# Optimization experiments

Hardware: AMD Instinct MI355X
Metric: run time of the kernel (lower is better)

Reference implementation:

```python
import jax, jax.numpy as jnp
import numpy as np

B, CIN, COUT, K, H, W = 16, 256, 256, 3, 64, 64
COND = 512


def setup_inputs() -> dict:
    key = jax.random.key(0)
    ks = jax.random.split(key, 10)
    X = jax.random.normal(ks[0], (B, CIN, H, W), dtype=jnp.float32)
    cond_v = jax.random.normal(ks[1], (B, COND), dtype=jnp.float32)
    # conv weight [O, I, kh, kw]
    conv_w = jax.random.normal(ks[2], (COUT, CIN, K, K), dtype=jnp.float32) / np.sqrt(CIN * K * K)
    w0 = jax.random.normal(ks[3], (COND, COND), dtype=jnp.float32) / np.sqrt(COND)
    b0 = jnp.zeros((COND,), dtype=jnp.float32)
    w1 = jax.random.normal(ks[4], (COND, COND), dtype=jnp.float32) / np.sqrt(COND)
    b1 = jnp.zeros((COND,), dtype=jnp.float32)
    w_out = jax.random.normal(ks[5], (CIN, COND), dtype=jnp.float32) / np.sqrt(COND)
    b_out = jnp.zeros((CIN,), dtype=jnp.float32)
    return {"X": X, "cond_v": cond_v, "conv_w": conv_w,
            "w0": w0, "b0": b0, "w1": w1, "b1": b1,
            "w_out": w_out, "b_out": b_out}


def reference(X, cond_v, conv_w, w0, b0, w1, b1, w_out, b_out):
    # proj_cond MLP: (Linear+SiLU) x depth, final Linear -> in_channels
    h = jax.nn.silu(cond_v @ w0.T + b0)
    h = jax.nn.silu(h @ w1.T + b1)
    scale = h @ w_out.T + b_out + 1.0          # [B, I]
    # modulate: bw[b,o,i,kh,kw] = w[o,i,kh,kw] * scale[b,i]
    bw = conv_w[None] * scale[:, None, :, None, None]
    # demodulate across (i, kh, kw)
    demod = jax.lax.rsqrt(jnp.sum(bw * bw, axis=(2, 3, 4)) + 1e-8)  # [B, O]
    bw = bw * demod[:, :, None, None, None]
    b, o, i, kh, kw = bw.shape
    # per-sample conv via grouped conv: x -> [1, B*I, H, W], w -> [B*O, I, kh, kw]
    x = X.reshape(1, b * i, X.shape[2], X.shape[3])
    w = bw.reshape(b * o, i, kh, kw)
    out = jax.lax.conv_general_dilated(
        x, w, window_strides=(1, 1), padding="SAME",
        feature_group_count=b,
        dimension_numbers=("NCHW", "OIHW", "NCHW"))
    return out.reshape(b, o, out.shape[2], out.shape[3])
```

## Files before the change

### kernel.cpp

```cpp
#include <hip/hip_runtime.h>
#include <hip/hip_bf16.h>
#include <cstdint>

#define NB 16
#define CI 256
#define CO 256
#define HH 64
#define WW 64
#define CC 512
#define HP 66
#define WP 66

typedef short short8 __attribute__((ext_vector_type(8)));
typedef float floatx4 __attribute__((ext_vector_type(4)));
typedef unsigned int uintx4 __attribute__((ext_vector_type(4)));

__device__ __forceinline__ void g2lds16(const void* g, void* l) {
  __builtin_amdgcn_global_load_lds((const __attribute__((address_space(1))) void*)g,
                                   (__attribute__((address_space(3))) void*)l, 16, 0, 0);
}

#define ASM_VMCNT0() do { asm volatile("s_waitcnt vmcnt(0)" ::: "memory"); \
                          __builtin_amdgcn_sched_barrier(0); } while (0)
#define ASM_VMCNT4() do { asm volatile("s_waitcnt vmcnt(4)" ::: "memory"); \
                          __builtin_amdgcn_sched_barrier(0); } while (0)
#define RAW_BAR() do { __builtin_amdgcn_sched_barrier(0);  \
                       __builtin_amdgcn_s_barrier();       \
                       __builtin_amdgcn_sched_barrier(0); } while (0)

template<int KD, int N, bool SILU, bool PLUSONE, int BJ>
__global__ void k_mlp(const float* __restrict__ in, const float* __restrict__ w,
                      const float* __restrict__ bias, float* __restrict__ out) {
  __shared__ float4 sin4[KD / 4];
  const int nb = N / BJ;
  int b = blockIdx.x / nb;
  int j = (blockIdx.x % nb) * BJ + threadIdx.x;
  const float4* in4 = reinterpret_cast<const float4*>(in + (size_t)b * KD);
  for (int k = threadIdx.x; k < KD / 4; k += BJ) sin4[k] = in4[k];
  __syncthreads();
  float acc = bias[j];
  const float4* wr = reinterpret_cast<const float4*>(w + (size_t)j * KD);
#pragma unroll 8
  for (int kk = 0; kk < KD / 4; ++kk) {
    float4 wv = wr[kk];
    float4 sv = sin4[kk];
    acc += wv.x * sv.x + wv.y * sv.y + wv.z * sv.z + wv.w * sv.w;
  }
  if (SILU) acc = acc / (1.0f + __expf(-acc));
  if (PLUSONE) acc += 1.0f;
  out[(size_t)b * N + j] = acc;
}

__global__ void k_repack(const float* __restrict__ cw, __hip_bfloat16* __restrict__ Wt,
                         float* __restrict__ wsq) {
  int gid = blockIdx.x * 256 + threadIdx.x;
  if (gid >= CO * CI) return;
  const float* p = cw + (size_t)gid * 9;
  float s = 0.0f;
#pragma unroll
  for (int t = 0; t < 9; ++t) {
    float v = p[t];
    s += v * v;
    Wt[(size_t)t * CO * CI + gid] = __float2bfloat16(v);
  }
  wsq[gid] = s;
}

__global__ void k_demod(const float* __restrict__ wsq, const float* __restrict__ scale,
                        float* __restrict__ demod) {
  __shared__ float s2[CI];
  int b = blockIdx.x;
  int o = threadIdx.x;
  float sv = scale[b * CI + o];
  s2[o] = sv * sv;
  __syncthreads();
  float acc = 0.0f;
  const float4* wr = reinterpret_cast<const float4*>(wsq + (size_t)o * CI);
  const float4* s4 = reinterpret_cast<const float4*>(s2);
#pragma unroll 8
  for (int i = 0; i < CI / 4; ++i) {
    float4 wv = wr[i];
    float4 sq = s4[i];
    acc += wv.x * sq.x + wv.y * sq.y + wv.z * sq.z + wv.w * sq.w;
  }
  demod[b * CO + o] = rsqrtf(acc + 1e-8f);
}

__global__ void k_scalex(const float* __restrict__ X, const float* __restrict__ scale,
                         __hip_bfloat16* __restrict__ Xs) {
  __shared__ float tile[64][68];
  __shared__ float ssc[64];
  int bid = blockIdx.x;
  int b = bid >> 8;
  int rem = bid & 255;
  int h = rem >> 2;
  int i0 = (rem & 3) * 64;
  int t = threadIdx.x;
  if (t < 64) ssc[t] = scale[b * CI + i0 + t];

  __hip_bfloat16* xs_img = Xs + (size_t)b * HP * WP * CI;
  uintx4 z = {0u, 0u, 0u, 0u};
  if (t < 16) {
    int px = (t >> 3) * 65;
    int sl = t & 7;
    *reinterpret_cast<uintx4*>(xs_img + (((size_t)(h + 1)) * WP + px) * CI + i0 + sl * 8) = z;
  }
  if (h == 0) {
    for (int u = t; u < 66 * 8; u += 256) {
      int px = u >> 3, sl = u & 7;
      *reinterpret_cast<uintx4*>(xs_img + ((size_t)px) * CI + i0 + sl * 8) = z;
    }
  }
  if (h == 63) {
    for (int u = t; u < 66 * 8; u += 256) {
      int px = u >> 3, sl = u & 7;
      *reinterpret_cast<uintx4*>(xs_img + ((size_t)65 * WP + px) * CI + i0 + sl * 8) = z;
    }
  }

  const float* src = X + (((size_t)b * CI + i0) * HH + h) * WW;
  int ii_base = t >> 4;
  int w4 = (t & 15) * 4;
#pragma unroll
  for (int r2 = 0; r2 < 4; ++r2) {
    int ii = r2 * 16 + ii_base;
    int key = ((ii >> 3) & 7) << 2;
    *reinterpret_cast<float4*>(&tile[ii][w4 ^ key]) =
        *reinterpret_cast<const float4*>(src + (size_t)ii * HH * WW + w4);
  }
  __syncthreads();
  int u = t & 7;
  int wl = t >> 3;
  int key = u << 2;
#pragma unroll
  for (int iter = 0; iter < 2; ++iter) {
    int w2 = wl + iter * 32;
    union { unsigned short us[8]; uintx4 v; } pk;
#pragma unroll
    for (int j = 0; j < 8; ++j) {
      int ii = u * 8 + j;
      float v = tile[ii][w2 ^ key] * ssc[ii];
      __hip_bfloat16 hb = __float2bfloat16(v);
      pk.us[j] = *reinterpret_cast<unsigned short*>(&hb);
    }
    *reinterpret_cast<uintx4*>(xs_img + (((size_t)(h + 1)) * WP + (w2 + 1)) * CI + i0 + u * 8) = pk.v;
  }
}

__global__ __launch_bounds__(512, 2)
void k_conv(const __hip_bfloat16* __restrict__ Xs, const __hip_bfloat16* __restrict__ Wt,
            const float* __restrict__ demod, float* __restrict__ out) {
  __shared__ __align__(16) char lds[55296 + 2 * 32768];
  char* sX  = lds;
  char* sA0 = lds + 55296;

  int wg = (blockIdx.x & 7) * 32 + (blockIdx.x >> 3);
  int b = wg >> 4;
  int ht = wg & 15;
  int h0 = ht * 4;

  int tid = threadIdx.x;
  int wv = tid >> 6;
  int lane = tid & 63;
  int lhi = lane >> 4;
  int llo = lane & 15;
  int wo = wv >> 1;
  int wpx = wv & 1;

  floatx4 acc[4][8];
#pragma unroll
  for (int m = 0; m < 4; ++m)
#pragma unroll
    for (int n = 0; n < 8; ++n) acc[m][n] = (floatx4){0.f, 0.f, 0.f, 0.f};

  int row_a[4], ra7[4];
#pragma unroll
  for (int m = 0; m < 4; ++m) { row_a[m] = wo * 64 + m * 16 + llo; ra7[m] = row_a[m] & 7; }

  const __hip_bfloat16* xs_img = Xs + (size_t)b * HP * WP * CI;

  for (int ic = 0; ic < 4; ++ic) {
    for (int j = wv; j < 54; j += 8) {
      int u = j * 64 + lane;
      int pr = u >> 3;
      int slot = lane & 7;
      int lr = pr / 72;
      int wp = pr - lr * 72;
      if (wp > 65) wp = 65;
      int isel = ic * 64 + ((slot ^ (pr & 7)) << 3);
      const __hip_bfloat16* src = xs_img + (((size_t)(h0 + lr) * WP + wp) * CI + isel);
      g2lds16(src, sX + j * 1024);
    }
    {
      const __hip_bfloat16* wbase = Wt + ic * 64;
#pragma unroll
      for (int jj = 0; jj < 4; ++jj) {
        int j = wv * 4 + jj;
        int row = j * 8 + (lane >> 3);
        int slot = lane & 7;
        int isel = (slot ^ (row & 7)) << 3;
        g2lds16(wbase + (size_t)row * CI + isel, sA0 + j * 1024);
      }
    }
    ASM_VMCNT0();
    RAW_BAR();

    for (int t = 0; t < 9; ++t) {
      char* sA = sA0 + (t & 1) * 32768;
      if (t < 8) {
        const __hip_bfloat16* wbase = Wt + (size_t)(t + 1) * CO * CI + ic * 64;
        char* dst = sA0 + ((t + 1) & 1) * 32768;
#pragma unroll
        for (int jj = 0; jj < 4; ++jj) {
          int j = wv * 4 + jj;
          int row = j * 8 + (lane >> 3);
          int slot = lane & 7;
          int isel = (slot ^ (row & 7)) << 3;
          g2lds16(wbase + (size_t)row * CI + isel, dst + j * 1024);
        }
        ASM_VMCNT4();
      } else {
        ASM_VMCNT0();
      }
      RAW_BAR();

      int kh = t / 3;
      int kw = t - kh * 3;
#pragma unroll
      for (int k32 = 0; k32 < 2; ++k32) {
        int kidx = k32 * 4 + lhi;
        short8 af[4];
#pragma unroll
        for (int m = 0; m < 4; ++m) {
          int addr = row_a[m] * 128 + ((kidx ^ ra7[m]) << 4);
          af[m] = *reinterpret_cast<const short8*>(sA + addr);
        }
#pragma unroll
        for (int n = 0; n < 8; ++n) {
          int stripe = wpx * 2 + (n >> 2) + kh;
          int px = (n & 3) * 16 + llo + kw;
          int prl = stripe * 72 + px;
          int addr = prl * 128 + ((kidx ^ (prl & 7)) << 4);
          short8 bq = *reinterpret_cast<const short8*>(sX + addr);
#pragma unroll
          for (int m = 0; m < 4; ++m)
            acc[m][n] = __builtin_amdgcn_mfma_f32_16x16x32_bf16(af[m], bq, acc[m][n], 0, 0, 0);
        }
      }
      RAW_BAR();
    }
  }

#pragma unroll
  for (int m = 0; m < 4; ++m) {
    int obase_o = wo * 64 + m * 16 + lhi * 4;
    float4 dmv = *reinterpret_cast<const float4*>(demod + (size_t)b * CO + obase_o);
#pragma unroll
    for (int j = 0; j < 4; ++j) {
      int o = obase_o + j;
      float dm = (j == 0) ? dmv.x : (j == 1) ? dmv.y : (j == 2) ? dmv.z : dmv.w;
      float* orow = out + (((size_t)b * CO + o) * HH + h0) * WW;
#pragma unroll
      for (int n = 0; n < 8; ++n) {
        int row = wpx * 2 + (n >> 2);
        int col = (n & 3) * 16 + llo;
        orow[(size_t)row * WW + col] = acc[m][n][j] * dm;
      }
    }
  }
}

extern "C" void kernel_launch(void* const* d_in, const int* in_sizes, int n_in,
                              void* d_out, int out_size, void* d_ws, size_t ws_size,
                              hipStream_t stream) {
  const float* X      = (const float*)d_in[0];
  const float* cond_v = (const float*)d_in[1];
  const float* conv_w = (const float*)d_in[2];
  const float* w0     = (const float*)d_in[3];
  const float* b0     = (const float*)d_in[4];
  const float* w1     = (const float*)d_in[5];
  const float* b1     = (const float*)d_in[6];
  const float* w_out  = (const float*)d_in[7];
  const float* b_out  = (const float*)d_in[8];
  float* out = (float*)d_out;

  char* ws = (char*)d_ws;
  const size_t XS_BYTES  = (size_t)NB * HP * WP * CI * 2;
  const size_t WT_BYTES  = (size_t)9 * CO * CI * 2;
  const size_t WSQ_BYTES = (size_t)CO * CI * 4;
  __hip_bfloat16* Xs = (__hip_bfloat16*)ws;
  __hip_bfloat16* Wt = (__hip_bfloat16*)(ws + XS_BYTES);
  float* wsq   = (float*)(ws + XS_BYTES + WT_BYTES);
  float* h0b   = (float*)(ws + XS_BYTES + WT_BYTES + WSQ_BYTES);
  float* h1b   = h0b + NB * CC;
  float* scale = h1b + NB * CC;
  float* demod = scale + NB * CI;

  k_repack<<<(CO * CI) / 256, 256, 0, stream>>>(conv_w, Wt, wsq);
  k_mlp<CC, CC, true, false, 128><<<NB * (CC / 128), 128, 0, stream>>>(cond_v, w0, b0, h0b);
  k_mlp<CC, CC, true, false, 128><<<NB * (CC / 128), 128, 0, stream>>>(h0b, w1, b1, h1b);
  k_mlp<CC, CI, false, true, 128><<<NB * (CI / 128), 128, 0, stream>>>(h1b, w_out, b_out, scale);
  k_demod<<<NB, CO, 0, stream>>>(wsq, scale, demod);
  k_scalex<<<NB * 64 * 4, 256, 0, stream>>>(X, scale, Xs);
  k_conv<<<NB * 16, 512, 0, stream>>>(Xs, Wt, demod, out);
}
```

Measured before the change: 135.9 us.

## Split conv over output-channel halves and double-buffer input tiles across 32-channel chunks

The conv kernel now launches twice as many 256-thread workgroups, each covering half of the output channels, and walks input channels in 32-wide chunks instead of 64. The X halo tile is double-buffered, and the next chunk's X is prefetched piecewise during the 9 tap iterations, so the per-chunk full drain and barrier before X reuse goes away. Weight tiles shrink to 8 KB double buffers. The aim is better load/compute overlap and more workgroups for occupancy. In exchange there are more barriers per MFMA (one k-step per tap instead of two), the X tile is reloaded by both output halves, and the XOR swizzle is dropped, which risks LDS bank conflicts.

```diff
diff --git a/kernel.cpp b/kernel.cpp
--- a/kernel.cpp
+++ b/kernel.cpp
@@ -22,7 +22,9 @@
 
 #define ASM_VMCNT0() do { asm volatile("s_waitcnt vmcnt(0)" ::: "memory"); \
                           __builtin_amdgcn_sched_barrier(0); } while (0)
-#define ASM_VMCNT4() do { asm volatile("s_waitcnt vmcnt(4)" ::: "memory"); \
+#define ASM_VMCNT2() do { asm volatile("s_waitcnt vmcnt(2)" ::: "memory"); \
+                          __builtin_amdgcn_sched_barrier(0); } while (0)
+#define ASM_VMCNT3() do { asm volatile("s_waitcnt vmcnt(3)" ::: "memory"); \
                           __builtin_amdgcn_sched_barrier(0); } while (0)
 #define RAW_BAR() do { __builtin_amdgcn_sched_barrier(0);  \
                        __builtin_amdgcn_s_barrier();       \
@@ -147,24 +149,27 @@
   }
 }
 
-__global__ __launch_bounds__(512, 2)
+__global__ __launch_bounds__(256, 2)
 void k_conv(const __hip_bfloat16* __restrict__ Xs, const __hip_bfloat16* __restrict__ Wt,
             const float* __restrict__ demod, float* __restrict__ out) {
-  __shared__ __align__(16) char lds[55296 + 2 * 32768];
-  char* sX  = lds;
-  char* sA0 = lds + 55296;
-
-  int wg = (blockIdx.x & 7) * 32 + (blockIdx.x >> 3);
-  int b = wg >> 4;
-  int ht = wg & 15;
+  __shared__ __align__(16) char lds[2 * 28672 + 2 * 8192];
+  char* sX0 = lds;
+  char* sA0 = lds + 57344;
+
+  int wg = (blockIdx.x & 7) * 64 + (blockIdx.x >> 3);
+  int b = wg >> 5;
+  int rem = wg & 31;
+  int ht = rem >> 1;
+  int ob = rem & 1;
   int h0 = ht * 4;
+  int o0 = ob * 128;
 
   int tid = threadIdx.x;
   int wv = tid >> 6;
   int lane = tid & 63;
   int lhi = lane >> 4;
   int llo = lane & 15;
-  int wo = wv >> 1;
+  int wo2 = wv >> 1;
   int wpx = wv & 1;
 
   floatx4 acc[4][8];
@@ -173,79 +178,72 @@
 #pragma unroll
     for (int n = 0; n < 8; ++n) acc[m][n] = (floatx4){0.f, 0.f, 0.f, 0.f};
 
-  int row_a[4], ra7[4];
-#pragma unroll
-  for (int m = 0; m < 4; ++m) { row_a[m] = wo * 64 + m * 16 + llo; ra7[m] = row_a[m] & 7; }
-
   const __hip_bfloat16* xs_img = Xs + (size_t)b * HP * WP * CI;
 
-  for (int ic = 0; ic < 4; ++ic) {
-    for (int j = wv; j < 54; j += 8) {
-      int u = j * 64 + lane;
-      int pr = u >> 3;
-      int slot = lane & 7;
-      int lr = pr / 72;
-      int wp = pr - lr * 72;
-      if (wp > 65) wp = 65;
-      int isel = ic * 64 + ((slot ^ (pr & 7)) << 3);
-      const __hip_bfloat16* src = xs_img + (((size_t)(h0 + lr) * WP + wp) * CI + isel);
-      g2lds16(src, sX + j * 1024);
-    }
-    {
-      const __hip_bfloat16* wbase = Wt + ic * 64;
-#pragma unroll
-      for (int jj = 0; jj < 4; ++jj) {
-        int j = wv * 4 + jj;
-        int row = j * 8 + (lane >> 3);
-        int slot = lane & 7;
-        int isel = (slot ^ (row & 7)) << 3;
-        g2lds16(wbase + (size_t)row * CI + isel, sA0 + j * 1024);
+  int xoff[7];
+#pragma unroll
+  for (int s = 0; s < 7; ++s) {
+    int j = wv + 4 * s;
+    int pr = 16 * j + (lane >> 2);
+    if (pr > 431) pr = 431;
+    int lr = pr / 72;
+    int wp = pr - lr * 72;
+    if (wp > 65) wp = 65;
+    xoff[s] = ((h0 + lr) * WP + wp) * CI + (lane & 3) * 8;
+  }
+  int a_off[2];
+#pragma unroll
+  for (int jj = 0; jj < 2; ++jj)
+    a_off[jj] = (o0 + 32 * wv + 16 * jj + (lane >> 2)) * CI + (lane & 3) * 8;
+
+#pragma unroll
+  for (int s = 0; s < 7; ++s)
+    g2lds16(xs_img + xoff[s], sX0 + (wv + 4 * s) * 1024);
+#pragma unroll
+  for (int jj = 0; jj < 2; ++jj)
+    g2lds16(Wt + a_off[jj], sA0 + (wv * 2 + jj) * 1024);
+  ASM_VMCNT0();
+  RAW_BAR();
+
+  for (int c = 0; c < 8; ++c) {
+    const char* xbuf = sX0 + (c & 1) * 28672;
+#pragma unroll
+    for (int t = 0; t < 9; ++t) {
+      int gt = c * 9 + t;
+      bool xiss = (t >= 2) && (c < 7);
+      if (xiss) {
+        int s = t - 2;
+        g2lds16(xs_img + xoff[s] + (c + 1) * 32,
+                sX0 + ((c + 1) & 1) * 28672 + (wv + 4 * s) * 1024);
       }
-    }
-    ASM_VMCNT0();
-    RAW_BAR();
-
-    for (int t = 0; t < 9; ++t) {
-      char* sA = sA0 + (t & 1) * 32768;
-      if (t < 8) {
-        const __hip_bfloat16* wbase = Wt + (size_t)(t + 1) * CO * CI + ic * 64;
-        char* dst = sA0 + ((t + 1) & 1) * 32768;
-#pragma unroll
-        for (int jj = 0; jj < 4; ++jj) {
-          int j = wv * 4 + jj;
-          int row = j * 8 + (lane >> 3);
-          int slot = lane & 7;
-          int isel = (slot ^ (row & 7)) << 3;
-          g2lds16(wbase + (size_t)row * CI + isel, dst + j * 1024);
-        }
-        ASM_VMCNT4();
+      if (gt < 71) {
+        int nt = (t == 8) ? 0 : t + 1;
+        int ncc = (t == 8) ? c + 1 : c;
+        const __hip_bfloat16* wb = Wt + (size_t)nt * CO * CI + ncc * 32;
+        char* ad = sA0 + ((gt + 1) & 1) * 8192;
+        g2lds16(wb + a_off[0], ad + (wv * 2 + 0) * 1024);
+        g2lds16(wb + a_off[1], ad + (wv * 2 + 1) * 1024);
+        if (xiss) { ASM_VMCNT3(); } else { ASM_VMCNT2(); }
       } else {
         ASM_VMCNT0();
       }
       RAW_BAR();
 
+      const char* sA = sA0 + (gt & 1) * 8192;
       int kh = t / 3;
       int kw = t - kh * 3;
-#pragma unroll
-      for (int k32 = 0; k32 < 2; ++k32) {
-        int kidx = k32 * 4 + lhi;
-        short8 af[4];
-#pragma unroll
-        for (int m = 0; m < 4; ++m) {
-          int addr = row_a[m] * 128 + ((kidx ^ ra7[m]) << 4);
-          af[m] = *reinterpret_cast<const short8*>(sA + addr);
-        }
-#pragma unroll
-        for (int n = 0; n < 8; ++n) {
-          int stripe = wpx * 2 + (n >> 2) + kh;
-          int px = (n & 3) * 16 + llo + kw;
-          int prl = stripe * 72 + px;
-          int addr = prl * 128 + ((kidx ^ (prl & 7)) << 4);
-          short8 bq = *reinterpret_cast<const short8*>(sX + addr);
-#pragma unroll
-          for (int m = 0; m < 4; ++m)
-            acc[m][n] = __builtin_amdgcn_mfma_f32_16x16x32_bf16(af[m], bq, acc[m][n], 0, 0, 0);
-        }
+      short8 af[4];
+#pragma unroll
+      for (int m = 0; m < 4; ++m)
+        af[m] = *reinterpret_cast<const short8*>(sA + (wo2 * 64 + m * 16 + llo) * 64 + lhi * 16);
+#pragma unroll
+      for (int n = 0; n < 8; ++n) {
+        int stripe = wpx * 2 + (n >> 2) + kh;
+        int px = (n & 3) * 16 + llo + kw;
+        short8 bq = *reinterpret_cast<const short8*>(xbuf + (stripe * 72 + px) * 64 + lhi * 16);
+#pragma unroll
+        for (int m = 0; m < 4; ++m)
+          acc[m][n] = __builtin_amdgcn_mfma_f32_16x16x32_bf16(af[m], bq, acc[m][n], 0, 0, 0);
       }
       RAW_BAR();
     }
@@ -253,7 +251,7 @@
 
 #pragma unroll
   for (int m = 0; m < 4; ++m) {
-    int obase_o = wo * 64 + m * 16 + lhi * 4;
+    int obase_o = o0 + wo2 * 64 + m * 16 + lhi * 4;
     float4 dmv = *reinterpret_cast<const float4*>(demod + (size_t)b * CO + obase_o);
 #pragma unroll
     for (int j = 0; j < 4; ++j) {
@@ -302,5 +300,5 @@
   k_mlp<CC, CI, false, true, 128><<<NB * (CI / 128), 128, 0, stream>>>(h1b, w_out, b_out, scale);
   k_demod<<<NB, CO, 0, stream>>>(wsq, scale, demod);
   k_scalex<<<NB * 64 * 4, 256, 0, stream>>>(X, scale, Xs);
-  k_conv<<<NB * 16, 512, 0, stream>>>(Xs, Wt, demod, out);
-}
+  k_conv<<<NB * 32, 256, 0, stream>>>(Xs, Wt, demod, out);
+}
```

After: 132.7 us. 2.4% less time.
